# Optimization experiments

Hardware: AMD Instinct MI355X
Metric: run time of the kernel (lower is better)

## Reference

```python
import jax, jax.numpy as jnp
import numpy as np

N_CLASS = 21
EPS = 1e-07


def setup_inputs() -> dict:
    key = jax.random.key(0)
    k1, k2 = jax.random.split(key)
    shape = (32, 512, 512)
    class_pred = jax.random.randint(k1, shape, 0, N_CLASS, dtype=jnp.int32)
    class_gt = jax.random.randint(k2, shape, 0, N_CLASS, dtype=jnp.int32)
    return {"class_pred": class_pred, "class_gt": class_gt}


def reference(class_pred, class_gt):
    # Single-pass histogram formulation of the original O(n_class) loop.
    pred = class_pred.reshape(-1)
    gt = class_gt.reshape(-1)
    # Per-class counts: bincount with fixed length (jit-compatible).
    pred_counts = jnp.bincount(pred, length=N_CLASS).astype(jnp.float32)
    gt_counts = jnp.bincount(gt, length=N_CLASS).astype(jnp.float32)
    # Intersection per class: count positions where pred == gt == i.
    # Route mismatches to an extra overflow bin (N_CLASS), then drop it.
    match_ids = jnp.where(pred == gt, pred, N_CLASS)
    intersection = jnp.bincount(match_ids, length=N_CLASS + 1)[:N_CLASS].astype(jnp.float32)
    union = pred_counts + gt_counts - intersection
    iou = (intersection + EPS) / (union + EPS)  # [n_class]
    return jnp.mean(iou)
```

## Files before the change

kernel.cpp:

```cpp
#include <hip/hip_runtime.h>

#define NC 21
#define NB (NC * NC)
#define NWAVES 8
#define HPAD 448
#define NBLK 512
#define NTHR 512
#define UNROLL 8

__global__ void __launch_bounds__(NTHR) zero_hist(unsigned* __restrict__ h) {
    int i = threadIdx.x;
    if (i < NB) h[i] = 0u;
}

__global__ void __launch_bounds__(NTHR) hist_kernel(const int* __restrict__ pred,
                                                    const int* __restrict__ gt,
                                                    unsigned* __restrict__ g_hist,
                                                    int n) {
    __shared__ unsigned h[NWAVES][HPAD];
    const int tid = threadIdx.x;
    const int wave = tid >> 6;

    #pragma unroll
    for (int i = tid; i < NWAVES * HPAD; i += NTHR) (&h[0][0])[i] = 0u;
    __syncthreads();

    const int n4 = n >> 2;
    const int4* __restrict__ p4 = (const int4*)pred;
    const int4* __restrict__ g4 = (const int4*)gt;
    const int stride = NBLK * NTHR;
    const int gidx = (int)blockIdx.x * NTHR + tid;

    int base = gidx;
    for (; base + (UNROLL - 1) * stride < n4; base += UNROLL * stride) {
        int4 pv[UNROLL], gv[UNROLL];
        #pragma unroll
        for (int k = 0; k < UNROLL; ++k) pv[k] = p4[base + k * stride];
        #pragma unroll
        for (int k = 0; k < UNROLL; ++k) gv[k] = g4[base + k * stride];
        #pragma unroll
        for (int k = 0; k < UNROLL; ++k) {
            atomicAdd(&h[wave][pv[k].x + NC * gv[k].x], 1u);
            atomicAdd(&h[wave][pv[k].y + NC * gv[k].y], 1u);
            atomicAdd(&h[wave][pv[k].z + NC * gv[k].z], 1u);
            atomicAdd(&h[wave][pv[k].w + NC * gv[k].w], 1u);
        }
    }
    for (; base < n4; base += stride) {
        int4 p = p4[base], g = g4[base];
        atomicAdd(&h[wave][p.x + NC * g.x], 1u);
        atomicAdd(&h[wave][p.y + NC * g.y], 1u);
        atomicAdd(&h[wave][p.z + NC * g.z], 1u);
        atomicAdd(&h[wave][p.w + NC * g.w], 1u);
    }
    for (int i = (n4 << 2) + gidx; i < n; i += stride) {
        atomicAdd(&h[wave][pred[i] + NC * gt[i]], 1u);
    }

    __syncthreads();
    for (int i = tid; i < NB; i += NTHR) {
        unsigned s = 0;
        #pragma unroll
        for (int w = 0; w < NWAVES; ++w) s += h[w][i];
        if (s) atomicAdd(&g_hist[i], s);
    }
}

__global__ void __launch_bounds__(64) miou_final(const unsigned* __restrict__ hist,
                                                 float* __restrict__ out) {
    const int lane = threadIdx.x;
    float iou = 0.0f;
    if (lane < NC) {
        float pc = 0.0f, gc = 0.0f;
        #pragma unroll
        for (int g = 0; g < NC; ++g) pc += (float)hist[lane + NC * g];
        #pragma unroll
        for (int p = 0; p < NC; ++p) gc += (float)hist[p + NC * lane];
        float inter = (float)hist[lane * (NC + 1)];
        float uni = pc + gc - inter;
        iou = (inter + 1e-7f) / (uni + 1e-7f);
    }
    for (int off = 32; off; off >>= 1) iou += __shfl_down(iou, off);
    if (lane == 0) out[0] = iou * (1.0f / 21.0f);
}

extern "C" void kernel_launch(void* const* d_in, const int* in_sizes, int n_in,
                              void* d_out, int out_size, void* d_ws, size_t ws_size,
                              hipStream_t stream) {
    const int* pred = (const int*)d_in[0];
    const int* gt   = (const int*)d_in[1];
    unsigned* g_hist = (unsigned*)d_ws;
    float* out = (float*)d_out;
    const int n = in_sizes[0];

    zero_hist<<<1, NTHR, 0, stream>>>(g_hist);
    hist_kernel<<<NBLK, NTHR, 0, stream>>>(pred, gt, g_hist, n);
    miou_final<<<1, 64, 0, stream>>>(g_hist, out);
}
```

Measured before the change: 98.27 us.

## Replace LDS atomic joint histogram with per-thread register class counters

After: 124.7 us. +26.9%, slower.

```diff
diff --git a/kernel.cpp b/kernel.cpp
--- a/kernel.cpp
+++ b/kernel.cpp
@@ -1,87 +1,122 @@
 #include <hip/hip_runtime.h>
 
 #define NC 21
-#define NB (NC * NC)
+#define NCNT 63
+#define NTHR 512
+#define NBLK 512
 #define NWAVES 8
-#define HPAD 448
-#define NBLK 512
-#define NTHR 512
-#define UNROLL 8
-
-__global__ void __launch_bounds__(NTHR) zero_hist(unsigned* __restrict__ h) {
-    int i = threadIdx.x;
-    if (i < NB) h[i] = 0u;
-}
+#define NPK 32
 
 __global__ void __launch_bounds__(NTHR) hist_kernel(const int* __restrict__ pred,
                                                     const int* __restrict__ gt,
-                                                    unsigned* __restrict__ g_hist,
+                                                    unsigned* __restrict__ partials,
                                                     int n) {
-    __shared__ unsigned h[NWAVES][HPAD];
-    const int tid = threadIdx.x;
-    const int wave = tid >> 6;
-
+    unsigned cnt[NCNT];
     #pragma unroll
-    for (int i = tid; i < NWAVES * HPAD; i += NTHR) (&h[0][0])[i] = 0u;
-    __syncthreads();
+    for (int i = 0; i < NCNT; ++i) cnt[i] = 0u;
 
     const int n4 = n >> 2;
     const int4* __restrict__ p4 = (const int4*)pred;
     const int4* __restrict__ g4 = (const int4*)gt;
     const int stride = NBLK * NTHR;
-    const int gidx = (int)blockIdx.x * NTHR + tid;
+    const int gidx = (int)blockIdx.x * NTHR + (int)threadIdx.x;
+
+#define PROC(pv_, gv_)                                                        \
+    {                                                                         \
+        const int p_ = (pv_), g_ = (gv_);                                     \
+        const unsigned e_ = (unsigned)(p_ == g_);                             \
+        _Pragma("unroll")                                                     \
+        for (int c = 0; c < NC; ++c) {                                        \
+            cnt[c]          += (unsigned)(p_ == c);                           \
+            cnt[NC + c]     += (unsigned)(g_ == c);                           \
+            cnt[2 * NC + c] += ((unsigned)(p_ == c)) & e_;                    \
+        }                                                                     \
+    }
 
     int base = gidx;
-    for (; base + (UNROLL - 1) * stride < n4; base += UNROLL * stride) {
-        int4 pv[UNROLL], gv[UNROLL];
+    for (; base + 3 * stride < n4; base += 4 * stride) {
+        int4 pv[4], gv[4];
         #pragma unroll
-        for (int k = 0; k < UNROLL; ++k) pv[k] = p4[base + k * stride];
+        for (int k = 0; k < 4; ++k) pv[k] = p4[base + k * stride];
         #pragma unroll
-        for (int k = 0; k < UNROLL; ++k) gv[k] = g4[base + k * stride];
+        for (int k = 0; k < 4; ++k) gv[k] = g4[base + k * stride];
         #pragma unroll
-        for (int k = 0; k < UNROLL; ++k) {
-            atomicAdd(&h[wave][pv[k].x + NC * gv[k].x], 1u);
-            atomicAdd(&h[wave][pv[k].y + NC * gv[k].y], 1u);
-            atomicAdd(&h[wave][pv[k].z + NC * gv[k].z], 1u);
-            atomicAdd(&h[wave][pv[k].w + NC * gv[k].w], 1u);
+        for (int k = 0; k < 4; ++k) {
+            PROC(pv[k].x, gv[k].x); PROC(pv[k].y, gv[k].y);
+            PROC(pv[k].z, gv[k].z); PROC(pv[k].w, gv[k].w);
         }
     }
     for (; base < n4; base += stride) {
         int4 p = p4[base], g = g4[base];
-        atomicAdd(&h[wave][p.x + NC * g.x], 1u);
-        atomicAdd(&h[wave][p.y + NC * g.y], 1u);
-        atomicAdd(&h[wave][p.z + NC * g.z], 1u);
-        atomicAdd(&h[wave][p.w + NC * g.w], 1u);
+        PROC(p.x, g.x); PROC(p.y, g.y); PROC(p.z, g.z); PROC(p.w, g.w);
     }
-    for (int i = (n4 << 2) + gidx; i < n; i += stride) {
-        atomicAdd(&h[wave][pred[i] + NC * gt[i]], 1u);
+    for (int i = (n4 << 2) + gidx; i < n; i += stride)
+        PROC(pred[i], gt[i]);
+#undef PROC
+
+    unsigned pk[NPK];
+    #pragma unroll
+    for (int i = 0; i < NPK; ++i) {
+        unsigned lo = cnt[2 * i];
+        unsigned hi = (2 * i + 1 < NCNT) ? cnt[2 * i + 1] : 0u;
+        pk[i] = lo | (hi << 16);
+    }
+    #pragma unroll
+    for (int i = 0; i < NPK; ++i) {
+        unsigned v = pk[i];
+        for (int off = 32; off; off >>= 1) v += __shfl_down(v, off);
+        pk[i] = v;
     }
 
+    __shared__ unsigned lds_pk[NWAVES][NPK];
+    const int lane = threadIdx.x & 63;
+    const int wav  = threadIdx.x >> 6;
+    if (lane == 0) {
+        #pragma unroll
+        for (int i = 0; i < NPK; ++i) lds_pk[wav][i] = pk[i];
+    }
     __syncthreads();
-    for (int i = tid; i < NB; i += NTHR) {
+
+    if (threadIdx.x < NPK) {
         unsigned s = 0;
         #pragma unroll
-        for (int w = 0; w < NWAVES; ++w) s += h[w][i];
-        if (s) atomicAdd(&g_hist[i], s);
+        for (int w = 0; w < NWAVES; ++w) s += lds_pk[w][threadIdx.x];
+        unsigned* outp = partials + (size_t)blockIdx.x * 64;
+        outp[2 * threadIdx.x] = s & 0xffffu;
+        if (2 * threadIdx.x + 1 < NCNT) outp[2 * threadIdx.x + 1] = s >> 16;
     }
 }
 
-__global__ void __launch_bounds__(64) miou_final(const unsigned* __restrict__ hist,
-                                                 float* __restrict__ out) {
-    const int lane = threadIdx.x;
+__global__ void __launch_bounds__(NTHR) reduce_miou(const unsigned* __restrict__ partials,
+                                                    float* __restrict__ out) {
+    __shared__ unsigned acc[8][64];
+    __shared__ float tot[64];
+    const int c  = threadIdx.x & 63;
+    const int bs = threadIdx.x >> 6;
+    unsigned s = 0;
+    #pragma unroll 8
+    for (int b = bs; b < NBLK; b += 8) s += partials[b * 64 + c];
+    acc[bs][c] = s;
+    __syncthreads();
+    if (threadIdx.x < 64) {
+        unsigned t = 0;
+        #pragma unroll
+        for (int w = 0; w < 8; ++w) t += acc[w][threadIdx.x];
+        tot[threadIdx.x] = (float)t;
+    }
+    __syncthreads();
     float iou = 0.0f;
-    if (lane < NC) {
-        float pc = 0.0f, gc = 0.0f;
-        #pragma unroll
-        for (int g = 0; g < NC; ++g) pc += (float)hist[lane + NC * g];
-        #pragma unroll
-        for (int p = 0; p < NC; ++p) gc += (float)hist[p + NC * lane];
-        float inter = (float)hist[lane * (NC + 1)];
-        float uni = pc + gc - inter;
-        iou = (inter + 1e-7f) / (uni + 1e-7f);
+    if (threadIdx.x < NC) {
+        float pc = tot[threadIdx.x];
+        float gc = tot[NC + threadIdx.x];
+        float it = tot[2 * NC + threadIdx.x];
+        float uni = pc + gc - it;
+        iou = (it + 1e-7f) / (uni + 1e-7f);
     }
-    for (int off = 32; off; off >>= 1) iou += __shfl_down(iou, off);
-    if (lane == 0) out[0] = iou * (1.0f / 21.0f);
+    if (threadIdx.x < 64) {
+        for (int off = 32; off; off >>= 1) iou += __shfl_down(iou, off);
+        if (threadIdx.x == 0) out[0] = iou * (1.0f / 21.0f);
+    }
 }
 
 extern "C" void kernel_launch(void* const* d_in, const int* in_sizes, int n_in,
@@ -89,11 +124,10 @@
                               hipStream_t stream) {
     const int* pred = (const int*)d_in[0];
     const int* gt   = (const int*)d_in[1];
-    unsigned* g_hist = (unsigned*)d_ws;
+    unsigned* partials = (unsigned*)d_ws;
     float* out = (float*)d_out;
     const int n = in_sizes[0];
 
-    zero_hist<<<1, NTHR, 0, stream>>>(g_hist);
-    hist_kernel<<<NBLK, NTHR, 0, stream>>>(pred, gt, g_hist, n);
-    miou_final<<<1, 64, 0, stream>>>(g_hist, out);
+    hist_kernel<<<NBLK, NTHR, 0, stream>>>(pred, gt, partials, n);
+    reduce_miou<<<1, NTHR, 0, stream>>>(partials, out);
 }
```
